# Kernel tuning notes

Measured on AMD Instinct MI355X. Metric: run time of the kernel, lower is better.

## Reference

```python
import jax, jax.numpy as jnp
import numpy as np

N_NODES = 80000
N_EDGES = 1280000
IN_CH = 128
OUT_CH = 32
HID = 2 * OUT_CH


def gcn_conv(x, W, b, src, dst, n_nodes):
    """PyG GCNConv with self-loops and symmetric normalization.
    out[i] = b + sum_{j->i} deg(j)^-1/2 deg(i)^-1/2 (x_j @ W)
    """
    loop = jnp.arange(n_nodes, dtype=src.dtype)
    s = jnp.concatenate([src, loop])  # [E+N]
    d = jnp.concatenate([dst, loop])  # [E+N]
    deg = jax.ops.segment_sum(jnp.ones_like(d, dtype=x.dtype), d,
                              num_segments=n_nodes)  # in-degree incl. self loop
    dinv = jnp.where(deg > 0, jax.lax.rsqrt(deg), 0.0)
    norm = dinv[s] * dinv[d]  # [E+N]
    h = x @ W  # [N, F_out] dense transform first (fewer flops when F_out < F_in)
    msg = h[s] * norm[:, None]  # [E+N, F_out] gather + scale
    out = jax.ops.segment_sum(msg, d, num_segments=n_nodes)  # scatter-add
    return out + b


def setup_inputs() -> dict:
    key = jax.random.key(0)
    k1, k2, k3, k4 = jax.random.split(key, 4)
    x = jax.random.normal(k1, (N_NODES, IN_CH), dtype=jnp.float32)
    edge_index = jax.random.randint(k2, (2, N_EDGES), 0, N_NODES, dtype=jnp.int64)
    W1 = jax.random.normal(k3, (IN_CH, HID), dtype=jnp.float32) / np.sqrt(IN_CH)
    b1 = jnp.zeros((HID,), dtype=jnp.float32)
    W2 = jax.random.normal(k4, (HID, OUT_CH), dtype=jnp.float32) / np.sqrt(HID)
    b2 = jnp.zeros((OUT_CH,), dtype=jnp.float32)
    return {"x": x, "edge_index": edge_index, "W1": W1, "b1": b1,
            "W2": W2, "b2": b2}


def reference(x, edge_index, W1, b1, W2, b2):
    src, dst = edge_index[0], edge_index[1]
    h = jax.nn.relu(gcn_conv(x, W1, b1, src, dst, N_NODES))
    return gcn_conv(h, W2, b2, src, dst, N_NODES)
```

## Files before the change

### kernel.cpp

```cpp
#include <hip/hip_runtime.h>
#include <hip/hip_fp16.h>

#define N_NODES 80000
#define N_EDGES 1280000
#define IN_CH 128
#define HID 64
#define OUT_CH 32

#define NBUCK 625
#define CAP 3072
#define BIN_BLOCKS 256

typedef float vf2 __attribute__((ext_vector_type(2)));
typedef float vf4 __attribute__((ext_vector_type(4)));
typedef short short8 __attribute__((ext_vector_type(8)));
typedef float floatx4 __attribute__((ext_vector_type(4)));

__device__ __forceinline__ unsigned bf16rn(float x) {
    unsigned u = __float_as_uint(x);
    return (u + 0x7FFFu + ((u >> 16) & 1u)) >> 16;
}
__device__ __forceinline__ unsigned packbf2(float a, float b) {
    return bf16rn(a) | (bf16rn(b) << 16);
}
__device__ __forceinline__ float hl(unsigned u) {
    return __half2float(__ushort_as_half((unsigned short)(u & 0xFFFFu)));
}
__device__ __forceinline__ float hh(unsigned u) {
    return __half2float(__ushort_as_half((unsigned short)(u >> 16)));
}
__device__ __forceinline__ unsigned pack2h(float a, float b) {
    return (unsigned)__half_as_ushort(__float2half_rn(a)) |
           ((unsigned)__half_as_ushort(__float2half_rn(b)) << 16);
}

__global__ __launch_bounds__(256) void k_bin_gemm1(
        const int* __restrict__ src, const int* __restrict__ dst,
        int* __restrict__ gcur, unsigned int* __restrict__ binned,
        const float* __restrict__ x, const float* __restrict__ W1,
        unsigned short* __restrict__ h1h) {
    __shared__ unsigned short smem_u[26112];
    int bid = blockIdx.x, t = threadIdx.x;
    if (bid < BIN_BLOCKS) {
        int* hist = (int*)smem_u;
        int* lcur = hist + NBUCK;
        const int chunk = N_EDGES / BIN_BLOCKS;
        int e0 = bid * chunk;
        int e1 = e0 + chunk;
        for (int i = t; i < NBUCK; i += 256) hist[i] = 0;
        __syncthreads();
        for (int e = e0 + t; e < e1; e += 256)
            atomicAdd(&hist[dst[e] >> 7], 1);
        __syncthreads();
        for (int i = t; i < NBUCK; i += 256) {
            int h = hist[i];
            lcur[i] = h ? atomicAdd(&gcur[i], h) : 0;
        }
        __syncthreads();
        for (int e = e0 + t; e < e1; e += 256) {
            int d = dst[e];
            int bk = d >> 7;
            int pos = atomicAdd(&lcur[bk], 1);
            if (pos < CAP)
                binned[(size_t)bk * CAP + pos] =
                    (unsigned int)src[e] | ((unsigned int)(d & 127) << 17);
        }
    } else {
        unsigned short* sX = smem_u;
        unsigned short* sWT = smem_u + 128 * 136;
        long long nb = (long long)(bid - BIN_BLOCKS) * 128;
        for (int it = 0; it < 16; ++it) {
            int idx = t + it * 256;
            int node = idx >> 5, k4 = (idx & 31) * 4;
            float4 v = *(const float4*)&x[(nb + node) * IN_CH + k4];
            unsigned u0 = packbf2(v.x, v.y), u1 = packbf2(v.z, v.w);
            *(uint2*)&sX[node * 136 + k4] = (uint2){u0, u1};
        }
        for (int it = 0; it < 8; ++it) {
            int idx = t + it * 256;
            int k = idx >> 4, c4 = (idx & 15) * 4;
            float4 w = *(const float4*)&W1[k * 64 + c4];
            sWT[(c4 + 0) * 136 + k] = (unsigned short)bf16rn(w.x);
            sWT[(c4 + 1) * 136 + k] = (unsigned short)bf16rn(w.y);
            sWT[(c4 + 2) * 136 + k] = (unsigned short)bf16rn(w.z);
            sWT[(c4 + 3) * 136 + k] = (unsigned short)bf16rn(w.w);
        }
        __syncthreads();
        int wv = t >> 6, lane = t & 63;
        int lm = lane & 15, q = lane >> 4;
        int m0 = wv * 32;
        floatx4 acc[2][4];
#pragma unroll
        for (int i = 0; i < 2; ++i)
#pragma unroll
            for (int j = 0; j < 4; ++j) acc[i][j] = (floatx4){0.f, 0.f, 0.f, 0.f};
#pragma unroll
        for (int kk = 0; kk < 128; kk += 32) {
            short8 a0 = *(short8*)&sX[(m0 + lm) * 136 + kk + q * 8];
            short8 a1 = *(short8*)&sX[(m0 + 16 + lm) * 136 + kk + q * 8];
#pragma unroll
            for (int ct = 0; ct < 4; ++ct) {
                short8 bfr = *(short8*)&sWT[(ct * 16 + lm) * 136 + kk + q * 8];
                acc[0][ct] = __builtin_amdgcn_mfma_f32_16x16x32_bf16(a0, bfr, acc[0][ct], 0, 0, 0);
                acc[1][ct] = __builtin_amdgcn_mfma_f32_16x16x32_bf16(a1, bfr, acc[1][ct], 0, 0, 0);
            }
        }
#pragma unroll
        for (int mt = 0; mt < 2; ++mt)
#pragma unroll
            for (int ct = 0; ct < 4; ++ct)
#pragma unroll
                for (int r = 0; r < 4; ++r) {
                    long long node = nb + m0 + mt * 16 + q * 4 + r;
                    int c = ct * 16 + lm;
                    h1h[node * 64 + c] = __half_as_ushort(__float2half_rn(acc[mt][ct][r]));
                }
    }
}

__global__ __launch_bounds__(256) void k_csr(const unsigned int* __restrict__ binned,
                                             const int* __restrict__ cnt,
                                             int* __restrict__ csr,
                                             int* __restrict__ rs, int* __restrict__ re,
                                             float* __restrict__ dinv) {
    __shared__ int deg[128];
    __shared__ int scan[128];
    __shared__ int cur[128];
    int bk = blockIdx.x, t = threadIdx.x;
    int n_e = min(cnt[bk], CAP);
    const unsigned int* eb = binned + (size_t)bk * CAP;
    if (t < 128) deg[t] = 0;
    __syncthreads();
    for (int i = t; i < n_e; i += 256) atomicAdd(&deg[eb[i] >> 17], 1);
    __syncthreads();
    if (t < 128) scan[t] = deg[t];
    __syncthreads();
    for (int off = 1; off < 128; off <<= 1) {
        int v = (t < 128 && t >= off) ? scan[t - off] : 0;
        __syncthreads();
        if (t < 128) scan[t] += v;
        __syncthreads();
    }
    if (t < 128) {
        int incl = scan[t];
        int s = incl - deg[t];
        cur[t] = s;
        int n = bk * 128 + t;
        int base = bk * CAP;
        rs[n] = base + s;
        re[n] = base + incl;
        dinv[n] = rsqrtf((float)(deg[t] + 1));
    }
    __syncthreads();
    for (int i = t; i < n_e; i += 256) {
        unsigned int p = eb[i];
        int dL = p >> 17;
        int pos = atomicAdd(&cur[dL], 1);
        csr[bk * CAP + pos] = (int)(p & 0x1FFFF);
    }
}

__global__ __launch_bounds__(256) void k_agg64(
        const unsigned int* __restrict__ h1u, const int* __restrict__ csr,
        const int* __restrict__ rs_, const int* __restrict__ re_,
        const float* __restrict__ dinv, const float* __restrict__ b1,
        const float* __restrict__ W2, unsigned int* __restrict__ g2u) {
    __shared__ float sW2[64 * 32];
    __shared__ float sB1[64];
    __shared__ float sH2[4][2][64];
    int t = threadIdx.x;
    for (int i = t * 2; i < 64 * 32; i += 512)
        *(vf2*)&sW2[i] = *(const vf2*)&W2[i];
    if (t < 32) *(vf2*)&sB1[t * 2] = *(const vf2*)&b1[t * 2];

    int wv = t >> 6, lane = t & 63;
    int nd = lane >> 5;
    int q  = (lane >> 4) & 1;
    int fo = lane & 15;
    long long n = (long long)blockIdx.x * 8 + wv * 2 + nd;
    int a = rs_[n], b = re_[n];
    float ax = 0.f, ay = 0.f, az = 0.f, aw = 0.f;
    int e = a + q;
    for (; e + 6 < b; e += 8) {
        int s0 = csr[e], s1 = csr[e + 2], s2 = csr[e + 4], s3 = csr[e + 6];
        uint2 u0 = *(const uint2*)&h1u[(size_t)s0 * 32 + 2 * fo]; float d0 = dinv[s0];
        uint2 u1 = *(const uint2*)&h1u[(size_t)s1 * 32 + 2 * fo]; float d1 = dinv[s1];
        uint2 u2 = *(const uint2*)&h1u[(size_t)s2 * 32 + 2 * fo]; float d2 = dinv[s2];
        uint2 u3 = *(const uint2*)&h1u[(size_t)s3 * 32 + 2 * fo]; float d3 = dinv[s3];
        ax += d0 * hl(u0.x); ay += d0 * hh(u0.x); az += d0 * hl(u0.y); aw += d0 * hh(u0.y);
        ax += d1 * hl(u1.x); ay += d1 * hh(u1.x); az += d1 * hl(u1.y); aw += d1 * hh(u1.y);
        ax += d2 * hl(u2.x); ay += d2 * hh(u2.x); az += d2 * hl(u2.y); aw += d2 * hh(u2.y);
        ax += d3 * hl(u3.x); ay += d3 * hh(u3.x); az += d3 * hl(u3.y); aw += d3 * hh(u3.y);
    }
    for (; e < b; e += 2) {
        int s = csr[e];
        uint2 u = *(const uint2*)&h1u[(size_t)s * 32 + 2 * fo];
        float d = dinv[s];
        ax += d * hl(u.x); ay += d * hh(u.x); az += d * hl(u.y); aw += d * hh(u.y);
    }
    ax += __shfl_down(ax, 16); ay += __shfl_down(ay, 16);
    az += __shfl_down(az, 16); aw += __shfl_down(aw, 16);
    __syncthreads();
    if (q == 0) {
        float dn = dinv[n];
        uint2 un = *(const uint2*)&h1u[(size_t)n * 32 + 2 * fo];
        ax += dn * hl(un.x); ay += dn * hh(un.x);
        az += dn * hl(un.y); aw += dn * hh(un.y);
        float4 bb = *(const float4*)&sB1[4 * fo];
        vf4 h2v = {fmaxf(dn * ax + bb.x, 0.f), fmaxf(dn * ay + bb.y, 0.f),
                   fmaxf(dn * az + bb.z, 0.f), fmaxf(dn * aw + bb.w, 0.f)};
        *(vf4*)&sH2[wv][nd][4 * fo] = h2v;
    }
    __syncthreads();
    int col = lane & 31;
    int nd2 = lane >> 5;
    const float* hrow = sH2[wv][nd2];
    float g = 0.f;
#pragma unroll
    for (int k = 0; k < 64; ++k) g += hrow[k] * sW2[k * 32 + col];
    float g1 = __shfl_down(g, 1);
    float g2v = __shfl_down(g, 2);
    float g3 = __shfl_down(g, 3);
    if ((lane & 3) == 0) {
        long long nn = (long long)blockIdx.x * 8 + wv * 2 + nd2;
        uint2 p = {pack2h(g, g1), pack2h(g2v, g3)};
        *(uint2*)&g2u[(size_t)nn * 16 + (col >> 1)] = p;
    }
}

__global__ __launch_bounds__(256) void k_agg32(
        const unsigned int* __restrict__ g2u, const int* __restrict__ csr,
        const int* __restrict__ rs_, const int* __restrict__ re_,
        const float* __restrict__ dinv, const float* __restrict__ b2,
        float* __restrict__ outp) {
    int n = blockIdx.x * 4 + (threadIdx.x >> 6);
    int lane = threadIdx.x & 63;
    int oc = lane >> 3, fo = lane & 7;
    int a = rs_[n], b = re_[n];
    float ax = 0.f, ay = 0.f, az = 0.f, aw = 0.f;
    int e = a + oc;
    for (; e + 8 < b; e += 16) {
        int s0 = csr[e], s1 = csr[e + 8];
        uint2 u0 = *(const uint2*)&g2u[(size_t)s0 * 16 + 2 * fo]; float d0 = dinv[s0];
        uint2 u1 = *(const uint2*)&g2u[(size_t)s1 * 16 + 2 * fo]; float d1 = dinv[s1];
        ax += d0 * hl(u0.x); ay += d0 * hh(u0.x);
        az += d0 * hl(u0.y); aw += d0 * hh(u0.y);
        ax += d1 * hl(u1.x); ay += d1 * hh(u1.x);
        az += d1 * hl(u1.y); aw += d1 * hh(u1.y);
    }
    for (; e < b; e += 8) {
        int s = csr[e];
        uint2 u = *(const uint2*)&g2u[(size_t)s * 16 + 2 * fo];
        float d = dinv[s];
        ax += d * hl(u.x); ay += d * hh(u.x);
        az += d * hl(u.y); aw += d * hh(u.y);
    }
    ax += __shfl_down(ax, 32); ay += __shfl_down(ay, 32);
    az += __shfl_down(az, 32); aw += __shfl_down(aw, 32);
    ax += __shfl_down(ax, 16); ay += __shfl_down(ay, 16);
    az += __shfl_down(az, 16); aw += __shfl_down(aw, 16);
    ax += __shfl_down(ax, 8);  ay += __shfl_down(ay, 8);
    az += __shfl_down(az, 8);  aw += __shfl_down(aw, 8);
    if (oc == 0) {
        float dn = dinv[n];
        uint2 un = *(const uint2*)&g2u[(size_t)n * 16 + 2 * fo];
        ax += dn * hl(un.x); ay += dn * hh(un.x);
        az += dn * hl(un.y); aw += dn * hh(un.y);
        float4 bb = *(const float4*)&b2[4 * fo];
        vf4 o = {dn * ax + bb.x, dn * ay + bb.y, dn * az + bb.z, dn * aw + bb.w};
        __builtin_nontemporal_store(o, (vf4*)&outp[(size_t)n * 32 + 4 * fo]);
    }
}

static inline size_t align256(size_t x) { return (x + 255) & ~(size_t)255; }

extern "C" void kernel_launch(void* const* d_in, const int* in_sizes, int n_in,
                              void* d_out, int out_size, void* d_ws, size_t ws_size,
                              hipStream_t stream) {
    const float* x  = (const float*)d_in[0];
    const int*   ei = (const int*)d_in[1];
    const float* W1 = (const float*)d_in[2];
    const float* b1 = (const float*)d_in[3];
    const float* W2 = (const float*)d_in[4];
    const float* b2 = (const float*)d_in[5];
    float* out = (float*)d_out;

    const int* src = ei;
    const int* dst = ei + N_EDGES;

    char* ws = (char*)d_ws;
    size_t off = 0;
    int* gcur = (int*)(ws + off);              off = align256(off + NBUCK * 4);
    unsigned int* binned = (unsigned int*)(ws + off);
                                               off = align256(off + (size_t)NBUCK * CAP * 4);
    int* csr = (int*)(ws + off);               off = align256(off + (size_t)NBUCK * CAP * 4);
    int* rs  = (int*)(ws + off);               off = align256(off + (size_t)N_NODES * 4);
    int* re  = (int*)(ws + off);               off = align256(off + (size_t)N_NODES * 4);
    float* dinv = (float*)(ws + off);          off = align256(off + (size_t)N_NODES * 4);
    unsigned short* h1h = (unsigned short*)(ws + off);
                                               off = align256(off + (size_t)N_NODES * 64 * 2);
    unsigned int* g2u = (unsigned int*)(ws + off);
                                               off = align256(off + (size_t)N_NODES * 16 * 4);

    (void)hipMemsetAsync(gcur, 0, NBUCK * 4, stream);
    k_bin_gemm1<<<BIN_BLOCKS + N_NODES / 128, 256, 0, stream>>>(src, dst, gcur, binned,
                                                                x, W1, h1h);
    k_csr<<<NBUCK, 256, 0, stream>>>(binned, gcur, csr, rs, re, dinv);
    k_agg64<<<N_NODES / 8, 256, 0, stream>>>((const unsigned int*)h1h, csr, rs, re,
                                             dinv, b1, W2, g2u);
    k_agg32<<<N_NODES / 4, 256, 0, stream>>>(g2u, csr, rs, re, dinv, b2, out);
}
```

Before: 204.9 us.

## Prescale features by source dinv and persist-wave agg64 with register-shuffle GEMV

Folds the source-side degree normalisation into the stored features: k_csr rescales h1 rows by dinv, and agg64 scales its output g2 by dn. The edge loops therefore no longer gather dinv[src] per edge. k_agg64 becomes a grid-stride kernel with one wave per node over a fixed wave count, removing shared-memory staging and barriers; the W2 product is done through lane shuffles. Row start and end are packed into an int2, and each node's self row is loaded early. The risk is an extra fp16 rounding on prescaled values and an extra read-modify-write pass over h1 inside k_csr.

```diff
diff --git a/kernel.cpp b/kernel.cpp
--- a/kernel.cpp
+++ b/kernel.cpp
@@ -10,6 +10,7 @@
 #define NBUCK 625
 #define CAP 3072
 #define BIN_BLOCKS 256
+#define AGG64_WAVES 8192
 
 typedef float vf2 __attribute__((ext_vector_type(2)));
 typedef float vf4 __attribute__((ext_vector_type(4)));
@@ -121,11 +122,13 @@
 __global__ __launch_bounds__(256) void k_csr(const unsigned int* __restrict__ binned,
                                              const int* __restrict__ cnt,
                                              int* __restrict__ csr,
-                                             int* __restrict__ rs, int* __restrict__ re,
-                                             float* __restrict__ dinv) {
+                                             int2* __restrict__ rse,
+                                             float* __restrict__ dinv,
+                                             unsigned int* __restrict__ h1u) {
     __shared__ int deg[128];
     __shared__ int scan[128];
     __shared__ int cur[128];
+    __shared__ float sdinv[128];
     int bk = blockIdx.x, t = threadIdx.x;
     int n_e = min(cnt[bk], CAP);
     const unsigned int* eb = binned + (size_t)bk * CAP;
@@ -147,9 +150,10 @@
         cur[t] = s;
         int n = bk * 128 + t;
         int base = bk * CAP;
-        rs[n] = base + s;
-        re[n] = base + incl;
-        dinv[n] = rsqrtf((float)(deg[t] + 1));
+        rse[n] = make_int2(base + s, base + incl);
+        float dv = rsqrtf((float)(deg[t] + 1));
+        dinv[n] = dv;
+        sdinv[t] = dv;
     }
     __syncthreads();
     for (int i = t; i < n_e; i += 256) {
@@ -158,102 +162,114 @@
         int pos = atomicAdd(&cur[dL], 1);
         csr[bk * CAP + pos] = (int)(p & 0x1FFFF);
     }
+    size_t rbase = (size_t)bk * 128 * 32;
+    for (int i = t; i < 128 * 16; i += 256) {
+        int row = i >> 4, c = i & 15;
+        uint2 u = *(uint2*)&h1u[rbase + (size_t)row * 32 + 2 * c];
+        float dv = sdinv[row];
+        u.x = pack2h(dv * hl(u.x), dv * hh(u.x));
+        u.y = pack2h(dv * hl(u.y), dv * hh(u.y));
+        *(uint2*)&h1u[rbase + (size_t)row * 32 + 2 * c] = u;
+    }
 }
 
 __global__ __launch_bounds__(256) void k_agg64(
         const unsigned int* __restrict__ h1u, const int* __restrict__ csr,
-        const int* __restrict__ rs_, const int* __restrict__ re_,
-        const float* __restrict__ dinv, const float* __restrict__ b1,
-        const float* __restrict__ W2, unsigned int* __restrict__ g2u) {
+        const int2* __restrict__ rse, const float* __restrict__ dinv,
+        const float* __restrict__ b1, const float* __restrict__ W2,
+        unsigned int* __restrict__ g2u) {
     __shared__ float sW2[64 * 32];
-    __shared__ float sB1[64];
-    __shared__ float sH2[4][2][64];
     int t = threadIdx.x;
     for (int i = t * 2; i < 64 * 32; i += 512)
         *(vf2*)&sW2[i] = *(const vf2*)&W2[i];
-    if (t < 32) *(vf2*)&sB1[t * 2] = *(const vf2*)&b1[t * 2];
-
-    int wv = t >> 6, lane = t & 63;
-    int nd = lane >> 5;
-    int q  = (lane >> 4) & 1;
-    int fo = lane & 15;
-    long long n = (long long)blockIdx.x * 8 + wv * 2 + nd;
-    int a = rs_[n], b = re_[n];
-    float ax = 0.f, ay = 0.f, az = 0.f, aw = 0.f;
-    int e = a + q;
-    for (; e + 6 < b; e += 8) {
-        int s0 = csr[e], s1 = csr[e + 2], s2 = csr[e + 4], s3 = csr[e + 6];
-        uint2 u0 = *(const uint2*)&h1u[(size_t)s0 * 32 + 2 * fo]; float d0 = dinv[s0];
-        uint2 u1 = *(const uint2*)&h1u[(size_t)s1 * 32 + 2 * fo]; float d1 = dinv[s1];
-        uint2 u2 = *(const uint2*)&h1u[(size_t)s2 * 32 + 2 * fo]; float d2 = dinv[s2];
-        uint2 u3 = *(const uint2*)&h1u[(size_t)s3 * 32 + 2 * fo]; float d3 = dinv[s3];
-        ax += d0 * hl(u0.x); ay += d0 * hh(u0.x); az += d0 * hl(u0.y); aw += d0 * hh(u0.y);
-        ax += d1 * hl(u1.x); ay += d1 * hh(u1.x); az += d1 * hl(u1.y); aw += d1 * hh(u1.y);
-        ax += d2 * hl(u2.x); ay += d2 * hh(u2.x); az += d2 * hl(u2.y); aw += d2 * hh(u2.y);
-        ax += d3 * hl(u3.x); ay += d3 * hh(u3.x); az += d3 * hl(u3.y); aw += d3 * hh(u3.y);
-    }
-    for (; e < b; e += 2) {
-        int s = csr[e];
-        uint2 u = *(const uint2*)&h1u[(size_t)s * 32 + 2 * fo];
-        float d = dinv[s];
-        ax += d * hl(u.x); ay += d * hh(u.x); az += d * hl(u.y); aw += d * hh(u.y);
-    }
-    ax += __shfl_down(ax, 16); ay += __shfl_down(ay, 16);
-    az += __shfl_down(az, 16); aw += __shfl_down(aw, 16);
-    __syncthreads();
-    if (q == 0) {
+    __syncthreads();
+
+    int lane = t & 63;
+    int q = lane >> 4, fo = lane & 15;
+    int col = lane & 31, khalf = lane >> 5;
+    float4 bb = *(const float4*)&b1[4 * fo];
+    int wave = blockIdx.x * 4 + (t >> 6);
+
+    for (int n = wave; n < N_NODES; n += AGG64_WAVES) {
+        int2 rb = rse[n];
         float dn = dinv[n];
         uint2 un = *(const uint2*)&h1u[(size_t)n * 32 + 2 * fo];
-        ax += dn * hl(un.x); ay += dn * hh(un.x);
-        az += dn * hl(un.y); aw += dn * hh(un.y);
-        float4 bb = *(const float4*)&sB1[4 * fo];
-        vf4 h2v = {fmaxf(dn * ax + bb.x, 0.f), fmaxf(dn * ay + bb.y, 0.f),
-                   fmaxf(dn * az + bb.z, 0.f), fmaxf(dn * aw + bb.w, 0.f)};
-        *(vf4*)&sH2[wv][nd][4 * fo] = h2v;
-    }
-    __syncthreads();
-    int col = lane & 31;
-    int nd2 = lane >> 5;
-    const float* hrow = sH2[wv][nd2];
-    float g = 0.f;
-#pragma unroll
-    for (int k = 0; k < 64; ++k) g += hrow[k] * sW2[k * 32 + col];
-    float g1 = __shfl_down(g, 1);
-    float g2v = __shfl_down(g, 2);
-    float g3 = __shfl_down(g, 3);
-    if ((lane & 3) == 0) {
-        long long nn = (long long)blockIdx.x * 8 + wv * 2 + nd2;
-        uint2 p = {pack2h(g, g1), pack2h(g2v, g3)};
-        *(uint2*)&g2u[(size_t)nn * 16 + (col >> 1)] = p;
+        int a = rb.x, b = rb.y;
+        float ax = 0.f, ay = 0.f, az = 0.f, aw = 0.f;
+        int e = a + q;
+        for (; e + 12 < b; e += 16) {
+            int s0 = csr[e], s1 = csr[e + 4], s2 = csr[e + 8], s3 = csr[e + 12];
+            uint2 u0 = *(const uint2*)&h1u[(size_t)s0 * 32 + 2 * fo];
+            uint2 u1 = *(const uint2*)&h1u[(size_t)s1 * 32 + 2 * fo];
+            uint2 u2 = *(const uint2*)&h1u[(size_t)s2 * 32 + 2 * fo];
+            uint2 u3 = *(const uint2*)&h1u[(size_t)s3 * 32 + 2 * fo];
+            ax += hl(u0.x); ay += hh(u0.x); az += hl(u0.y); aw += hh(u0.y);
+            ax += hl(u1.x); ay += hh(u1.x); az += hl(u1.y); aw += hh(u1.y);
+            ax += hl(u2.x); ay += hh(u2.x); az += hl(u2.y); aw += hh(u2.y);
+            ax += hl(u3.x); ay += hh(u3.x); az += hl(u3.y); aw += hh(u3.y);
+        }
+        for (; e < b; e += 4) {
+            int s = csr[e];
+            uint2 u = *(const uint2*)&h1u[(size_t)s * 32 + 2 * fo];
+            ax += hl(u.x); ay += hh(u.x); az += hl(u.y); aw += hh(u.y);
+        }
+        ax += __shfl_down(ax, 32); ay += __shfl_down(ay, 32);
+        az += __shfl_down(az, 32); aw += __shfl_down(aw, 32);
+        ax += __shfl_down(ax, 16); ay += __shfl_down(ay, 16);
+        az += __shfl_down(az, 16); aw += __shfl_down(aw, 16);
+        ax += hl(un.x); ay += hh(un.x); az += hl(un.y); aw += hh(un.y);
+        ax = fmaxf(dn * ax + bb.x, 0.f);
+        ay = fmaxf(dn * ay + bb.y, 0.f);
+        az = fmaxf(dn * az + bb.z, 0.f);
+        aw = fmaxf(dn * aw + bb.w, 0.f);
+        float g = 0.f;
+#pragma unroll
+        for (int si = 0; si < 8; ++si) {
+            int srcl = khalf * 8 + si;
+            float h0 = __shfl(ax, srcl), h1v = __shfl(ay, srcl);
+            float h2v = __shfl(az, srcl), h3v = __shfl(aw, srcl);
+            int k0 = khalf * 32 + si * 4;
+            g += h0 * sW2[(k0 + 0) * 32 + col];
+            g += h1v * sW2[(k0 + 1) * 32 + col];
+            g += h2v * sW2[(k0 + 2) * 32 + col];
+            g += h3v * sW2[(k0 + 3) * 32 + col];
+        }
+        g += __shfl_down(g, 32);
+        g *= dn;
+        float g1 = __shfl_down(g, 1);
+        float g2v = __shfl_down(g, 2);
+        float g3v = __shfl_down(g, 3);
+        if (lane < 32 && (lane & 3) == 0) {
+            uint2 p = {pack2h(g, g1), pack2h(g2v, g3v)};
+            *(uint2*)&g2u[(size_t)n * 16 + (col >> 1)] = p;
+        }
     }
 }
 
 __global__ __launch_bounds__(256) void k_agg32(
         const unsigned int* __restrict__ g2u, const int* __restrict__ csr,
-        const int* __restrict__ rs_, const int* __restrict__ re_,
-        const float* __restrict__ dinv, const float* __restrict__ b2,
-        float* __restrict__ outp) {
+        const int2* __restrict__ rse, const float* __restrict__ dinv,
+        const float* __restrict__ b2, float* __restrict__ outp) {
     int n = blockIdx.x * 4 + (threadIdx.x >> 6);
     int lane = threadIdx.x & 63;
     int oc = lane >> 3, fo = lane & 7;
-    int a = rs_[n], b = re_[n];
+    int2 rb = rse[n];
+    float dn = dinv[n];
+    uint2 un = *(const uint2*)&g2u[(size_t)n * 16 + 2 * fo];
+    int a = rb.x, b = rb.y;
     float ax = 0.f, ay = 0.f, az = 0.f, aw = 0.f;
     int e = a + oc;
     for (; e + 8 < b; e += 16) {
         int s0 = csr[e], s1 = csr[e + 8];
-        uint2 u0 = *(const uint2*)&g2u[(size_t)s0 * 16 + 2 * fo]; float d0 = dinv[s0];
-        uint2 u1 = *(const uint2*)&g2u[(size_t)s1 * 16 + 2 * fo]; float d1 = dinv[s1];
-        ax += d0 * hl(u0.x); ay += d0 * hh(u0.x);
-        az += d0 * hl(u0.y); aw += d0 * hh(u0.y);
-        ax += d1 * hl(u1.x); ay += d1 * hh(u1.x);
-        az += d1 * hl(u1.y); aw += d1 * hh(u1.y);
+        uint2 u0 = *(const uint2*)&g2u[(size_t)s0 * 16 + 2 * fo];
+        uint2 u1 = *(const uint2*)&g2u[(size_t)s1 * 16 + 2 * fo];
+        ax += hl(u0.x); ay += hh(u0.x); az += hl(u0.y); aw += hh(u0.y);
+        ax += hl(u1.x); ay += hh(u1.x); az += hl(u1.y); aw += hh(u1.y);
     }
     for (; e < b; e += 8) {
         int s = csr[e];
         uint2 u = *(const uint2*)&g2u[(size_t)s * 16 + 2 * fo];
-        float d = dinv[s];
-        ax += d * hl(u.x); ay += d * hh(u.x);
-        az += d * hl(u.y); aw += d * hh(u.y);
+        ax += hl(u.x); ay += hh(u.x); az += hl(u.y); aw += hh(u.y);
     }
     ax += __shfl_down(ax, 32); ay += __shfl_down(ay, 32);
     az += __shfl_down(az, 32); aw += __shfl_down(aw, 32);
@@ -262,10 +278,8 @@
     ax += __shfl_down(ax, 8);  ay += __shfl_down(ay, 8);
     az += __shfl_down(az, 8);  aw += __shfl_down(aw, 8);
     if (oc == 0) {
-        float dn = dinv[n];
-        uint2 un = *(const uint2*)&g2u[(size_t)n * 16 + 2 * fo];
-        ax += dn * hl(un.x); ay += dn * hh(un.x);
-        az += dn * hl(un.y); aw += dn * hh(un.y);
+        ax += hl(un.x); ay += hh(un.x);
+        az += hl(un.y); aw += hh(un.y);
         float4 bb = *(const float4*)&b2[4 * fo];
         vf4 o = {dn * ax + bb.x, dn * ay + bb.y, dn * az + bb.z, dn * aw + bb.w};
         __builtin_nontemporal_store(o, (vf4*)&outp[(size_t)n * 32 + 4 * fo]);
@@ -294,8 +308,7 @@
     unsigned int* binned = (unsigned int*)(ws + off);
                                                off = align256(off + (size_t)NBUCK * CAP * 4);
     int* csr = (int*)(ws + off);               off = align256(off + (size_t)NBUCK * CAP * 4);
-    int* rs  = (int*)(ws + off);               off = align256(off + (size_t)N_NODES * 4);
-    int* re  = (int*)(ws + off);               off = align256(off + (size_t)N_NODES * 4);
+    int2* rse = (int2*)(ws + off);             off = align256(off + (size_t)N_NODES * 8);
     float* dinv = (float*)(ws + off);          off = align256(off + (size_t)N_NODES * 4);
     unsigned short* h1h = (unsigned short*)(ws + off);
                                                off = align256(off + (size_t)N_NODES * 64 * 2);
@@ -305,8 +318,9 @@
     (void)hipMemsetAsync(gcur, 0, NBUCK * 4, stream);
     k_bin_gemm1<<<BIN_BLOCKS + N_NODES / 128, 256, 0, stream>>>(src, dst, gcur, binned,
                                                                 x, W1, h1h);
-    k_csr<<<NBUCK, 256, 0, stream>>>(binned, gcur, csr, rs, re, dinv);
-    k_agg64<<<N_NODES / 8, 256, 0, stream>>>((const unsigned int*)h1h, csr, rs, re,
-                                             dinv, b1, W2, g2u);
-    k_agg32<<<N_NODES / 4, 256, 0, stream>>>(g2u, csr, rs, re, dinv, b2, out);
-}
+    k_csr<<<NBUCK, 256, 0, stream>>>(binned, gcur, csr, rse, dinv,
+                                     (unsigned int*)h1h);
+    k_agg64<<<AGG64_WAVES / 4, 256, 0, stream>>>((const unsigned int*)h1h, csr, rse,
+                                                 dinv, b1, W2, g2u);
+    k_agg32<<<N_NODES / 4, 256, 0, stream>>>(g2u, csr, rse, dinv, b2, out);
+}
```

New measurement: 223.8 us. +9.2%, slower.
